# Optimization experiments

Hardware: AMD Instinct MI355X
Metric: run time of the kernel (lower is better)

## Reference

```python
import jax, jax.numpy as jnp
import numpy as np

H = W = 1024
CHUNK = 32  # rows per chunk in the column EDT pass (keeps intermediate at 32*H*W floats)


def setup_inputs() -> dict:
    key = jax.random.key(0)
    k1, k2 = jax.random.split(key)
    preds = jax.random.randint(k1, (H, W), 0, 2).astype(jnp.float32)
    targets = jax.random.randint(k2, (H, W), 0, 2).astype(jnp.float32)
    return {"preds": preds, "targets": targets}


def _edges(seg):
    # morphological erosion via 3x3 box conv, threshold at 9 == kernel.numel()
    s = seg[None, None]  # (1,1,H,W)
    kern = jnp.ones((1, 1, 3, 3), seg.dtype)
    conv = jax.lax.conv_general_dilated(s, kern, (1, 1), ((1, 1), (1, 1)))
    eroded = (conv[0, 0] == 9.0).astype(seg.dtype)
    return seg - eroded


def _edt(edges):
    # exact Euclidean distance transform: distance to nearest zero of (1 - edges),
    # i.e. nearest pixel where edges == 1.  Separable exact algorithm:
    #   1) per-row 1D distance to nearest feature (via cummax/cummin scans)
    #   2) per-column lower envelope min_k g2[k,j] + (i-k)^2 (chunked brute force)
    feat = (1.0 - edges) == 0.0
    Hh, Ww = edges.shape
    BIG = jnp.float32(1e6)
    col = jnp.arange(Ww, dtype=jnp.float32)
    left = col - jax.lax.cummax(jnp.where(feat, col, -BIG), axis=1)
    right = jax.lax.cummin(jnp.where(feat, col, BIG), axis=1, reverse=True) - col
    g = jnp.minimum(jnp.minimum(left, right), BIG)  # row-wise 1D distance
    g2 = g * g  # (H,W) squared row distances
    rows = jnp.arange(Hh, dtype=jnp.float32)

    def chunk(ic):  # ic: (CHUNK,) target row indices
        # (CHUNK, H, W): g2[k,j] + (i-k)^2, min over source row k
        d = g2[None, :, :] + (ic[:, None, None] - rows[None, :, None]) ** 2
        return jnp.min(d, axis=1)  # (CHUNK, W)

    D2 = jax.lax.map(chunk, rows.reshape(-1, CHUNK)).reshape(Hh, Ww)
    return jnp.sqrt(D2)


def reference(preds, targets):
    pred_edges = _edges(preds)
    target_edges = _edges(targets)
    # scipy EDT ran on detached CPU copies -> no gradient through the DTs
    pred_dt = jax.lax.stop_gradient(_edt(pred_edges))
    target_dt = jax.lax.stop_gradient(_edt(target_edges))
    pred_err = target_edges * pred_dt
    target_err = pred_edges * target_dt
    loss = (jnp.mean(pred_err) + jnp.mean(target_err)) / 2.0
    return jax.nn.sigmoid(loss)
```

## Files before the change

### kernel.cpp

```cpp
#include <hip/hip_runtime.h>
#include <math.h>


#define HW 1024
#define WIN 8
#define RPB 128
#define KROWS (RPB + 2 * WIN)
#define HS_STRIDE 17
#define NC 146
#define NW 130
#define NCHUNK ((NC + NW) * 8)

__device__ inline int edge_at(const float* __restrict__ seg, int k, int j)
{
    if ((unsigned)k >= (unsigned)HW || (unsigned)j >= (unsigned)HW) return 0;
    if (seg[k * HW + j] == 0.f) return 0;
    bool all9 = true;
    #pragma unroll
    for (int dy = -1; dy <= 1; ++dy)
        #pragma unroll
        for (int dx = -1; dx <= 1; ++dx) {
            const int kk = k + dy, jj = j + dx;
            const float v = ((unsigned)kk < (unsigned)HW && (unsigned)jj < (unsigned)HW)
                            ? seg[kk * HW + jj] : 0.f;
            all9 = all9 && (v != 0.f);
        }
    return all9 ? 0 : 1;
}

__global__ __launch_bounds__(256)
void k_main(const float* __restrict__ pred, const float* __restrict__ targ,
            float* __restrict__ partial)
{
    const int t  = threadIdx.x;
    const int j0 = blockIdx.x * 16;
    const int i0 = blockIdx.y * RPB;
    const int mc = blockIdx.z;
    const float* __restrict__ segc = mc ? targ : pred;
    const float* __restrict__ segw = mc ? pred : targ;

    __shared__ alignas(16) unsigned char sbytes[NCHUNK];
    __shared__ unsigned s_m[NC + NW];
    __shared__ float hs[KROWS * HS_STRIDE];
    __shared__ unsigned short esb[RPB];
    __shared__ float wsum[4];

    const int W0 = j0 - 8;

    for (int idx = t; idx < NCHUNK; idx += 256) {
        const int  isW = idx >= NC * 8;
        const int  rel = isW ? idx - NC * 8 : idx;
        const int  row = rel >> 3, c4 = rel & 7;
        const int  gr  = isW ? (i0 - 1 + row) : (i0 - 9 + row);
        const int  c   = W0 + c4 * 4;
        float4 v = make_float4(0.f, 0.f, 0.f, 0.f);
        if ((unsigned)gr < (unsigned)HW && (unsigned)c <= 1020u) {
            const float* __restrict__ base = isW ? segw : segc;
            v = *(const float4*)&base[gr * HW + c];
        }
        const unsigned by = (unsigned)(v.x != 0.f) | ((unsigned)(v.y != 0.f) << 1)
                          | ((unsigned)(v.z != 0.f) << 2) | ((unsigned)(v.w != 0.f) << 3);
        sbytes[idx] = (unsigned char)by;
    }
    __syncthreads();

    for (int rowi = t; rowi < NC + NW; rowi += 256) {
        const uint2 u = *(const uint2*)&sbytes[rowi * 8];
        unsigned r = 0;
        const unsigned wq[2] = {u.x, u.y};
        #pragma unroll
        for (int q = 0; q < 2; ++q) {
            const unsigned x = wq[q] & 0x0F0F0F0Fu;
            const unsigned y = x | (x >> 4);
            const unsigned h16 = (y & 0xFFu) | (((y >> 16) & 0xFFu) << 8);
            r |= h16 << (16 * q);
        }
        s_m[rowi] = r;
    }
    __syncthreads();

    if (t < RPB) {
        const unsigned sA = s_m[NC + t], sB = s_m[NC + t + 1], sC = s_m[NC + t + 2];
        const unsigned va = sA & sB & sC;
        const unsigned er = va & (va << 1) & (va >> 1);
        const unsigned edge = sB & ~er;
        esb[t] = (unsigned short)((edge >> 8) & 0xFFFFu);
    }
    if (t < KROWS) {
        const int kr = i0 - WIN + t;
        float* __restrict__ hrow = &hs[t * HS_STRIDE];
        if ((unsigned)kr < (unsigned)HW) {
            const unsigned sA = s_m[t], sB = s_m[t + 1], sC = s_m[t + 2];
            const unsigned va = sA & sB & sC;
            const unsigned er = va & (va << 1) & (va >> 1);
            const unsigned edge = (sB & ~er) & 0x7FFFFFFEu;
            const float krk = (float)(kr * kr);
            #pragma unroll
            for (int jc = 0; jc < 16; ++jc) {
                const int p = 8 + jc;
                const unsigned mle = edge & ((1u << (p + 1)) - 1u);
                const unsigned mge = edge >> p;
                int g = 1 << 20;
                if (mle) g = p - (31 - __clz(mle));
                if (mge) g = min(g, __ffs(mge) - 1);
                hrow[jc] = (g < (1 << 20)) ? fmaf((float)g, (float)g, krk) : 1e30f;
            }
        } else {
            #pragma unroll
            for (int jc = 0; jc < 16; ++jc) hrow[jc] = 1e30f;
        }
    }
    __syncthreads();

    const int jj = t & 15;
    const int iw = t >> 4;
    float lsum = 0.f;

    #pragma unroll
    for (int g = 0; g < 2; ++g) {
        const int ib = i0 + iw * 8 + g * 4;
        const int kkS = iw * 8 + g * 4;
        float b0 = 3e38f, b1 = 3e38f, b2 = 3e38f, b3 = 3e38f;
        float kf = (float)(ib - WIN);
        const float m0 = -2.f * (float)(ib);
        const float m1 = -2.f * (float)(ib + 1);
        const float m2 = -2.f * (float)(ib + 2);
        const float m3 = -2.f * (float)(ib + 3);
        #pragma unroll
        for (int kk = kkS; kk < kkS + 2 * WIN + 4; ++kk) {
            const float hvv = hs[kk * HS_STRIDE + jj];
            b0 = fminf(b0, fmaf(m0, kf, hvv));
            b1 = fminf(b1, fmaf(m1, kf, hvv));
            b2 = fminf(b2, fmaf(m2, kf, hvv));
            b3 = fminf(b3, fmaf(m3, kf, hvv));
            kf += 1.f;
        }
        const int sLo = max(0, ib - WIN);
        const int sHi = min(HW - 1, ib + WIN + 3);
        float bs[4] = {b0, b1, b2, b3};
        #pragma unroll
        for (int w = 0; w < 4; ++w) {
            const int i = ib + w;
            float D2 = (float)(i * i) + bs[w];
            const int dl = i - sLo + 1, dr = sHi + 1 - i;
            const bool need = (D2 > 64.f) ||
                              ((sLo > 0) && (D2 > (float)(dl * dl))) ||
                              ((sHi < HW - 1) && (D2 > (float)(dr * dr)));
            if (need) {
                const int jg = j0 + jj;
                float bb = 1e6f - (float)jg;
                bb = bb * bb;
                for (int k = 0; k < HW; ++k) {
                    const float rowt = (float)((i - k) * (i - k));
                    if (rowt >= bb) continue;
                    for (int d = 0; d < HW; ++d) {
                        const float dd = rowt + (float)(d * d);
                        if (dd >= bb) break;
                        if (edge_at(segc, k, jg - d) || edge_at(segc, k, jg + d)) {
                            bb = dd; break;
                        }
                    }
                }
                D2 = bb;
            }
            const unsigned wbit = (esb[i - i0] >> jj) & 1u;
            lsum += wbit ? sqrtf(D2) : 0.f;
        }
    }

    #pragma unroll
    for (int off = 32; off > 0; off >>= 1) lsum += __shfl_down(lsum, off);
    if ((t & 63) == 0) wsum[t >> 6] = lsum;
    __syncthreads();
    if (t == 0) {
        const int bid = blockIdx.x + 64 * (blockIdx.y + 8 * blockIdx.z);
        partial[bid] = wsum[0] + wsum[1] + wsum[2] + wsum[3];
    }
}

__global__ __launch_bounds__(256)
void k_fin(const float* __restrict__ partial, float* __restrict__ out)
{
    const int t = threadIdx.x;
    float s = partial[t] + partial[t + 256] + partial[t + 512] + partial[t + 768];
    #pragma unroll
    for (int off = 32; off > 0; off >>= 1) s += __shfl_down(s, off);
    __shared__ float w[4];
    if ((t & 63) == 0) w[t >> 6] = s;
    __syncthreads();
    if (t == 0) {
        const float tot = w[0] + w[1] + w[2] + w[3];
        const float loss = tot * (1.f / (2.f * 1024.f * 1024.f));
        out[0] = 1.f / (1.f + expf(-loss));
    }
}

extern "C" void kernel_launch(void* const* d_in, const int* in_sizes, int n_in,
                              void* d_out, int out_size, void* d_ws, size_t ws_size,
                              hipStream_t stream)
{
    const float* preds   = (const float*)d_in[0];
    const float* targets = (const float*)d_in[1];
    float* out = (float*)d_out;

    float* partial = (float*)d_ws;

    dim3 gM(HW / 16, HW / RPB, 2);
    k_main<<<gM, 256, 0, stream>>>(preds, targets, partial);

    k_fin<<<1, 256, 0, stream>>>(partial, out);
}
```

Baseline: 72.07 us.

## Halve rows per block and pack row masks with wave shuffles

Rows per block drop from 128 to 64, which doubles the grid to 2048 blocks and gives each thread 4 output rows instead of 8, so more blocks can be spread across the GPU. The byte staging buffer and its second pass are removed: each group of 8 lanes combines its nibbles into a 32-bit row mask with xor shuffles and writes it straight to shared memory, which cuts one shared-memory round trip and one barrier. The cost is a larger halo, since the overhead rows become a bigger share of each block's loads. The partial-sum count and the final reduction are updated to match the new grid.

```diff
diff --git a/kernel.cpp b/kernel.cpp
--- a/kernel.cpp
+++ b/kernel.cpp
@@ -4,12 +4,13 @@
 
 #define HW 1024
 #define WIN 8
-#define RPB 128
+#define RPB 64
 #define KROWS (RPB + 2 * WIN)
 #define HS_STRIDE 17
-#define NC 146
-#define NW 130
-#define NCHUNK ((NC + NW) * 8)
+#define NC (RPB + 18)
+#define NW (RPB + 2)
+#define NROWS (NC + NW)
+#define NSLOT (NROWS * 8)
 
 __device__ inline int edge_at(const float* __restrict__ seg, int k, int j)
 {
@@ -39,43 +40,37 @@
     const float* __restrict__ segc = mc ? targ : pred;
     const float* __restrict__ segw = mc ? pred : targ;
 
-    __shared__ alignas(16) unsigned char sbytes[NCHUNK];
-    __shared__ unsigned s_m[NC + NW];
+    __shared__ unsigned s_m[NROWS];
     __shared__ float hs[KROWS * HS_STRIDE];
     __shared__ unsigned short esb[RPB];
     __shared__ float wsum[4];
 
     const int W0 = j0 - 8;
 
-    for (int idx = t; idx < NCHUNK; idx += 256) {
-        const int  isW = idx >= NC * 8;
-        const int  rel = isW ? idx - NC * 8 : idx;
-        const int  row = rel >> 3, c4 = rel & 7;
-        const int  gr  = isW ? (i0 - 1 + row) : (i0 - 9 + row);
-        const int  c   = W0 + c4 * 4;
-        float4 v = make_float4(0.f, 0.f, 0.f, 0.f);
-        if ((unsigned)gr < (unsigned)HW && (unsigned)c <= 1020u) {
-            const float* __restrict__ base = isW ? segw : segc;
-            v = *(const float4*)&base[gr * HW + c];
-        }
-        const unsigned by = (unsigned)(v.x != 0.f) | ((unsigned)(v.y != 0.f) << 1)
-                          | ((unsigned)(v.z != 0.f) << 2) | ((unsigned)(v.w != 0.f) << 3);
-        sbytes[idx] = (unsigned char)by;
-    }
-    __syncthreads();
-
-    for (int rowi = t; rowi < NC + NW; rowi += 256) {
-        const uint2 u = *(const uint2*)&sbytes[rowi * 8];
-        unsigned r = 0;
-        const unsigned wq[2] = {u.x, u.y};
-        #pragma unroll
-        for (int q = 0; q < 2; ++q) {
-            const unsigned x = wq[q] & 0x0F0F0F0Fu;
-            const unsigned y = x | (x >> 4);
-            const unsigned h16 = (y & 0xFFu) | (((y >> 16) & 0xFFu) << 8);
-            r |= h16 << (16 * q);
-        }
-        s_m[rowi] = r;
+    #pragma unroll
+    for (int it = 0; it < 5; ++it) {
+        const int idx = t + it * 256;
+        unsigned partm = 0;
+        int row = -1;
+        if (idx < NSLOT) {
+            row = idx >> 3;
+            const int c4 = idx & 7;
+            const int isW = row >= NC;
+            const int gr  = isW ? (i0 - 1 + (row - NC)) : (i0 - 9 + row);
+            const int c   = W0 + c4 * 4;
+            float4 v = make_float4(0.f, 0.f, 0.f, 0.f);
+            if ((unsigned)gr < (unsigned)HW && (unsigned)c <= 1020u) {
+                const float* __restrict__ base = isW ? segw : segc;
+                v = *(const float4*)&base[gr * HW + c];
+            }
+            const unsigned by = (unsigned)(v.x != 0.f) | ((unsigned)(v.y != 0.f) << 1)
+                              | ((unsigned)(v.z != 0.f) << 2) | ((unsigned)(v.w != 0.f) << 3);
+            partm = by << (4 * c4);
+        }
+        partm |= __shfl_xor(partm, 1);
+        partm |= __shfl_xor(partm, 2);
+        partm |= __shfl_xor(partm, 4);
+        if (idx < NSLOT && (t & 7) == 0) s_m[row] = partm;
     }
     __syncthreads();
 
@@ -115,11 +110,9 @@
     const int jj = t & 15;
     const int iw = t >> 4;
     float lsum = 0.f;
-
-    #pragma unroll
-    for (int g = 0; g < 2; ++g) {
-        const int ib = i0 + iw * 8 + g * 4;
-        const int kkS = iw * 8 + g * 4;
+    {
+        const int ib = i0 + iw * 4;
+        const int kkS = iw * 4;
         float b0 = 3e38f, b1 = 3e38f, b2 = 3e38f, b3 = 3e38f;
         float kf = (float)(ib - WIN);
         const float m0 = -2.f * (float)(ib);
@@ -173,7 +166,7 @@
     if ((t & 63) == 0) wsum[t >> 6] = lsum;
     __syncthreads();
     if (t == 0) {
-        const int bid = blockIdx.x + 64 * (blockIdx.y + 8 * blockIdx.z);
+        const int bid = blockIdx.x + 64 * (blockIdx.y + 16 * blockIdx.z);
         partial[bid] = wsum[0] + wsum[1] + wsum[2] + wsum[3];
     }
 }
@@ -182,7 +175,9 @@
 void k_fin(const float* __restrict__ partial, float* __restrict__ out)
 {
     const int t = threadIdx.x;
-    float s = partial[t] + partial[t + 256] + partial[t + 512] + partial[t + 768];
+    float s = 0.f;
+    #pragma unroll
+    for (int q = 0; q < 8; ++q) s += partial[t + q * 256];
     #pragma unroll
     for (int off = 32; off > 0; off >>= 1) s += __shfl_down(s, off);
     __shared__ float w[4];
```

Measured after the change: 72.36 us. About the same (+0.4%).
